# Optimization experiments

Hardware: AMD Instinct MI355X
Metric: run time of the kernel (lower is better)

Reference implementation:

```python
import jax, jax.numpy as jnp
import numpy as np

B, T, I, H, L, O = 256, 336, 16, 512, 256, 10


def setup_inputs() -> dict:
    key = jax.random.key(0)
    ks = jax.random.split(key, 24)
    n = lambda k, s, sc=1.0: jax.random.normal(k, s, dtype=jnp.float32) * sc
    mask = lambda k, s: (jax.random.uniform(k, s) > 0.5).astype(jnp.float32) * 2.0  # dropout p=0.5
    return {
        "x": n(ks[0], (B, T, I)),
        # dropout masks (inverted-dropout scaling already applied)
        "drop_x": mask(ks[1], (B, T, I)),
        "drop_h": mask(ks[2], (B, H)),
        "drop_l": mask(ks[3], (B, L)),
        # BayesianLSTM variational params + reparameterization noise
        "wih_mu": n(ks[4], (I, 4 * H), 0.05), "wih_rho": jnp.full((I, 4 * H), -5.0, jnp.float32), "eps_wih": n(ks[5], (I, 4 * H)),
        "whh_mu": n(ks[6], (H, 4 * H), 0.05), "whh_rho": jnp.full((H, 4 * H), -5.0, jnp.float32), "eps_whh": n(ks[7], (H, 4 * H)),
        "b_mu": n(ks[8], (4 * H,), 0.05), "b_rho": jnp.full((4 * H,), -5.0, jnp.float32), "eps_b": n(ks[9], (4 * H,)),
        # BayesianLinear variational params + noise (weight is [out, in])
        "blw_mu": n(ks[10], (L, H), 0.05), "blw_rho": jnp.full((L, H), -5.0, jnp.float32), "eps_blw": n(ks[11], (L, H)),
        "blb_mu": n(ks[12], (L,), 0.05), "blb_rho": jnp.full((L,), -5.0, jnp.float32), "eps_blb": n(ks[13], (L,)),
        # final deterministic linear, no bias
        "lin_w": n(ks[14], (O, L), 0.05),
    }


def _forward(x, drop_x, drop_h, drop_l,
             wih_mu, wih_rho, eps_wih, whh_mu, whh_rho, eps_whh,
             b_mu, b_rho, eps_b, blw_mu, blw_rho, eps_blw,
             blb_mu, blb_rho, eps_blb, lin_w):
    sp = jax.nn.softplus
    # sample weights: w = mu + softplus(rho) * eps
    Wih = wih_mu + sp(wih_rho) * eps_wih        # [I, 4H]
    Whh = whh_mu + sp(whh_rho) * eps_whh        # [H, 4H]
    b = b_mu + sp(b_rho) * eps_b                # [4H]
    BLW = blw_mu + sp(blw_rho) * eps_blw        # [L, H]
    BLb = blb_mu + sp(blb_rho) * eps_blb        # [L]

    xd = x * drop_x                             # dropout on input
    # precompute input-to-gate projection for all timesteps: [B, T, 4H]
    xg = jnp.einsum('bti,ig->btg', xd, Wih) + b

    def step(carry, xg_t):
        h, c = carry
        gates = xg_t + h @ Whh                  # [B, 4H]
        i, f, g, o = jnp.split(gates, 4, axis=-1)
        i = jax.nn.sigmoid(i)
        f = jax.nn.sigmoid(f)
        g = jnp.tanh(g)
        o = jax.nn.sigmoid(o)
        c = f * c + i * g
        h = o * jnp.tanh(c)
        return (h, c), h

    h0 = jnp.zeros((x.shape[0], Whh.shape[0]), x.dtype)
    (_, _), hs = jax.lax.scan(step, (h0, h0), jnp.swapaxes(xg, 0, 1))  # hs: [T, B, H]
    hidden_seq = jnp.swapaxes(hs, 0, 1)         # blitz returns batch-major [B, T, H]
    # faithful to lstm_out.view(sequence_length, len(x), hidden_dim)[-1] (reshape, not transpose)
    last = hidden_seq.reshape(T, x.shape[0], -1)[-1]    # [B, H]

    y = jax.nn.relu((last * drop_h) @ BLW.T + BLb)      # Bayesian linear + ReLU
    return (y * drop_l) @ lin_w.T                       # final linear, no bias


def reference(x, drop_x, drop_h, drop_l,
              wih_mu, wih_rho, eps_wih, whh_mu, whh_rho, eps_whh,
              b_mu, b_rho, eps_b, blw_mu, blw_rho, eps_blw,
              blb_mu, blb_rho, eps_blb, lin_w):
    return _forward(x, drop_x, drop_h, drop_l,
                    wih_mu, wih_rho, eps_wih, whh_mu, whh_rho, eps_whh,
                    b_mu, b_rho, eps_b, blw_mu, blw_rho, eps_blw,
                    blb_mu, blb_rho, eps_blb, lin_w)
```

## Files before the change

### kernel.cpp

```cpp
#include <hip/hip_runtime.h>
#include <hip/hip_fp16.h>

#define T_STEPS 336
#define NWG 32

typedef unsigned long long u64;

__device__ float g_h[337 * 512];
__device__ float g_blw[256 * 512];
__device__ float g_blb[256];
__device__ u64   g_hh[2][512];

__device__ __forceinline__ float softplus_f(float x) {
  return (x > 20.f) ? x : log1pf(__expf(x));
}
__device__ __forceinline__ float sigmoid_f(float x) {
  return 1.f / (1.f + __expf(-x));
}
__device__ __forceinline__ float tanh_f(float x) {
  x = fminf(fmaxf(x, -15.f), 15.f);
  float e = __expf(-2.f * x);
  return (1.f - e) / (1.f + e);
}

__global__ __launch_bounds__(256) void prep_kernel(
    const float* __restrict__ blw_mu, const float* __restrict__ blw_rho, const float* __restrict__ eps_blw,
    const float* __restrict__ blb_mu, const float* __restrict__ blb_rho, const float* __restrict__ eps_blb)
{
  const int bid = blockIdx.x, tid = threadIdx.x;
  if (bid < 512) {
    const int e = bid * 256 + tid;
    g_blw[e] = blw_mu[e] + softplus_f(blw_rho[e]) * eps_blw[e];
  } else {
    g_blb[tid] = blb_mu[tid] + softplus_f(blb_rho[tid]) * eps_blb[tid];
    u64* p = &g_hh[0][0];
    #pragma unroll
    for (int q = 0; q < 4; ++q)
      __hip_atomic_store(p + q * 256 + tid, 0ULL, __ATOMIC_RELAXED,
                         __HIP_MEMORY_SCOPE_AGENT);
  }
}

__global__ __launch_bounds__(512) void lstm_kernel(
    const float* __restrict__ x, const float* __restrict__ drop_x,
    const float* __restrict__ wih_mu, const float* __restrict__ wih_rho, const float* __restrict__ eps_wih,
    const float* __restrict__ b_mu, const float* __restrict__ b_rho, const float* __restrict__ eps_b,
    const float* __restrict__ whh_mu, const float* __restrict__ whh_rho, const float* __restrict__ eps_whh)
{
  const int r = blockIdx.x;
  const int tid = threadIdx.x;
  const int cl = tid & 63;
  const int seg = tid >> 6;
  const int gate = cl >> 4, kl = cl & 15;
  const int col = gate * 512 + r * 16 + kl;
  const int row0 = seg * 64;

  __shared__ float  xd[336 * 16];
  __shared__ __half hs16[512];
  __shared__ float  part[2][8][64];

  for (int e = tid; e < 5376; e += 512) {
    const int src = 255 * 5376 + e;
    xd[e] = x[src] * drop_x[src];
  }

  float w[64];
  #pragma unroll
  for (int j = 0; j < 64; ++j) {
    const int idx = (row0 + j) * 2048 + col;
    w[j] = whh_mu[idx] + softplus_f(whh_rho[idx]) * eps_whh[idx];
  }

  float wih[16];
  float bias = 0.f;
  if (tid < 64) {
    bias = b_mu[col] + softplus_f(b_rho[col]) * eps_b[col];
    #pragma unroll
    for (int i = 0; i < 16; ++i) {
      const int idx = i * 2048 + col;
      wih[i] = wih_mu[idx] + softplus_f(wih_rho[idx]) * eps_wih[idx];
    }
  }
  __syncthreads();

  auto xg_at = [&](int t) -> float {
    const float4* xr = (const float4*)(xd + t * 16);
    float4 x0 = xr[0], x1 = xr[1], x2 = xr[2], x3 = xr[3];
    float s0 = fmaf(x0.x, wih[0], bias);
    s0 = fmaf(x0.y, wih[1], s0); s0 = fmaf(x0.z, wih[2], s0); s0 = fmaf(x0.w, wih[3], s0);
    float s1 = x1.x * wih[4];
    s1 = fmaf(x1.y, wih[5], s1); s1 = fmaf(x1.z, wih[6], s1); s1 = fmaf(x1.w, wih[7], s1);
    float s2 = x2.x * wih[8];
    s2 = fmaf(x2.y, wih[9], s2); s2 = fmaf(x2.z, wih[10], s2); s2 = fmaf(x2.w, wih[11], s2);
    float s3 = x3.x * wih[12];
    s3 = fmaf(x3.y, wih[13], s3); s3 = fmaf(x3.z, wih[14], s3); s3 = fmaf(x3.w, wih[15], s3);
    return (s0 + s1) + (s2 + s3);
  };

  float c = 0.f;
  float xgv = (tid < 64) ? xg_at(0) : 0.f;

  for (int t = 0; t < T_STEPS; ++t) {
    const int p = t & 1;

    {
      const u64* slot = &g_hh[p][tid];
      u64 v;
      int it = 0;
      for (;;) {
        v = __hip_atomic_load(slot, __ATOMIC_RELAXED, __HIP_MEMORY_SCOPE_AGENT);
        if ((unsigned)(v >> 32) == (unsigned)t) break;
        if (++it > (1 << 20)) break;
      }
      hs16[tid] = __float2half(__uint_as_float((unsigned)v));
    }

    float a0 = 0.f, a1 = 0.f, a2 = 0.f, a3 = 0.f;
    const float4* hv = (const float4*)(hs16 + row0);
    #pragma unroll
    for (int jj = 0; jj < 8; ++jj) {
      float4 q = hv[jj];
      const __half2* hp = (const __half2*)&q;
      float2 f0 = __half22float2(hp[0]);
      float2 f1 = __half22float2(hp[1]);
      float2 f2 = __half22float2(hp[2]);
      float2 f3 = __half22float2(hp[3]);
      a0 = fmaf(f0.x, w[8 * jj],     a0);
      a1 = fmaf(f0.y, w[8 * jj + 1], a1);
      a2 = fmaf(f1.x, w[8 * jj + 2], a2);
      a3 = fmaf(f1.y, w[8 * jj + 3], a3);
      a0 = fmaf(f2.x, w[8 * jj + 4], a0);
      a1 = fmaf(f2.y, w[8 * jj + 5], a1);
      a2 = fmaf(f3.x, w[8 * jj + 6], a2);
      a3 = fmaf(f3.y, w[8 * jj + 7], a3);
    }
    part[p][seg][cl] = (a0 + a1) + (a2 + a3);
    __syncthreads();

    if (tid < 64) {
      float g = xgv
              + ((part[p][0][tid] + part[p][1][tid]) + (part[p][2][tid] + part[p][3][tid]))
              + ((part[p][4][tid] + part[p][5][tid]) + (part[p][6][tid] + part[p][7][tid]));
      const bool is_g = (gate == 2);
      float xin = is_g ? 2.f * fminf(fmaxf(g, -15.f), 15.f) : g;
      float s = sigmoid_f(xin);
      float act = is_g ? 2.f * s - 1.f : s;
      float vi = __shfl(act, kl);
      float vf = __shfl(act, kl + 16);
      float vg = __shfl(act, kl + 32);
      float vo = __shfl(act, kl + 48);
      if (tid < 16) {
        c = vf * c + vi * vg;
        float h = vo * tanh_f(c);
        const int idx = r * 16 + tid;
        u64 pv = (((u64)(unsigned)(t + 1)) << 32) | (u64)__float_as_uint(h);
        __hip_atomic_store(&g_hh[(t + 1) & 1][idx], pv,
                           __ATOMIC_RELAXED, __HIP_MEMORY_SCOPE_AGENT);
        g_h[(t + 1) * 512 + idx] = h;
      }
      if (t + 1 < T_STEPS) xgv = xg_at(t + 1);
    }
  }
}

__global__ __launch_bounds__(256) void head_kernel(
    const float* __restrict__ drop_h, const float* __restrict__ drop_l,
    const float* __restrict__ lin_w, float* __restrict__ out)
{
  const int j = blockIdx.x, tid = threadIdx.x;
  __shared__ float hd[512];
  __shared__ float y[256];

  for (int k = tid; k < 512; k += 256)
    hd[k] = g_h[(81 + j) * 512 + k] * drop_h[j * 512 + k];
  __syncthreads();

  {
    const int l = tid;
    float acc = g_blb[l];
    const float* wrow = g_blw + l * 512;
    #pragma unroll 8
    for (int k = 0; k < 512; ++k) acc = fmaf(hd[k], wrow[k], acc);
    acc = fmaxf(acc, 0.f);
    y[l] = acc * drop_l[j * 256 + l];
  }
  __syncthreads();

  if (tid < 10) {
    float acc = 0.f;
    const float* lrow = lin_w + tid * 256;
    #pragma unroll 8
    for (int l = 0; l < 256; ++l) acc = fmaf(y[l], lrow[l], acc);
    out[j * 10 + tid] = acc;
  }
}

extern "C" void kernel_launch(void* const* d_in, const int* in_sizes, int n_in,
                              void* d_out, int out_size, void* d_ws, size_t ws_size,
                              hipStream_t stream) {
  const float* x        = (const float*)d_in[0];
  const float* drop_x   = (const float*)d_in[1];
  const float* drop_h   = (const float*)d_in[2];
  const float* drop_l   = (const float*)d_in[3];
  const float* wih_mu   = (const float*)d_in[4];
  const float* wih_rho  = (const float*)d_in[5];
  const float* eps_wih  = (const float*)d_in[6];
  const float* whh_mu   = (const float*)d_in[7];
  const float* whh_rho  = (const float*)d_in[8];
  const float* eps_whh  = (const float*)d_in[9];
  const float* b_mu     = (const float*)d_in[10];
  const float* b_rho    = (const float*)d_in[11];
  const float* eps_b    = (const float*)d_in[12];
  const float* blw_mu   = (const float*)d_in[13];
  const float* blw_rho  = (const float*)d_in[14];
  const float* eps_blw  = (const float*)d_in[15];
  const float* blb_mu   = (const float*)d_in[16];
  const float* blb_rho  = (const float*)d_in[17];
  const float* eps_blb  = (const float*)d_in[18];
  const float* lin_w    = (const float*)d_in[19];

  prep_kernel<<<513, 256, 0, stream>>>(blw_mu, blw_rho, eps_blw,
                                       blb_mu, blb_rho, eps_blb);

  lstm_kernel<<<NWG, 512, 0, stream>>>(x, drop_x,
                                       wih_mu, wih_rho, eps_wih,
                                       b_mu, b_rho, eps_b,
                                       whh_mu, whh_rho, eps_whh);

  head_kernel<<<256, 256, 0, stream>>>(drop_h, drop_l, lin_w, (float*)d_out);
}
```

Before: 732.0 us.

## Pipeline spin-wait polling in inline asm and fold BLW sampling into LSTM

Replaces the scalar atomic-load spin loop with hand-written GCN assembly that keeps three outstanding global loads in flight, so each poll iteration overlaps memory latency instead of serialising load-compare. It also moves the BayesianLinear weight sampling from a large separate prep launch into the LSTM kernel's prologue, shrinking the init kernel to a single block. The inline asm clobbers fixed registers and uses cache-bypass loads, which adds fragility and extra memory traffic during polling.

```diff
diff --git a/kernel.cpp b/kernel.cpp
--- a/kernel.cpp
+++ b/kernel.cpp
@@ -23,29 +23,67 @@
   return (1.f - e) / (1.f + e);
 }
 
-__global__ __launch_bounds__(256) void prep_kernel(
-    const float* __restrict__ blw_mu, const float* __restrict__ blw_rho, const float* __restrict__ eps_blw,
-    const float* __restrict__ blb_mu, const float* __restrict__ blb_rho, const float* __restrict__ eps_blb)
+__device__ __forceinline__ unsigned poll_slot(const u64* slot, unsigned t) {
+  unsigned lo;
+  asm volatile(
+    "s_mov_b32 s22, 0x40000\n\t"
+    "global_load_dwordx2 v[60:61], %[p], off sc1\n\t"
+    "global_load_dwordx2 v[62:63], %[p], off sc1\n\t"
+    "global_load_dwordx2 v[64:65], %[p], off sc1\n\t"
+    "POLL%=:\n\t"
+    "s_sub_u32 s22, s22, 1\n\t"
+    "s_cbranch_scc1 DA%=\n\t"
+    "s_waitcnt vmcnt(2)\n\t"
+    "v_cmp_eq_u32 vcc, %[t], v61\n\t"
+    "s_not_b64 s[20:21], vcc\n\t"
+    "s_cbranch_scc0 DA%=\n\t"
+    "global_load_dwordx2 v[60:61], %[p], off sc1\n\t"
+    "s_waitcnt vmcnt(2)\n\t"
+    "v_cmp_eq_u32 vcc, %[t], v63\n\t"
+    "s_not_b64 s[20:21], vcc\n\t"
+    "s_cbranch_scc0 DB%=\n\t"
+    "global_load_dwordx2 v[62:63], %[p], off sc1\n\t"
+    "s_waitcnt vmcnt(2)\n\t"
+    "v_cmp_eq_u32 vcc, %[t], v65\n\t"
+    "s_not_b64 s[20:21], vcc\n\t"
+    "s_cbranch_scc0 DC%=\n\t"
+    "global_load_dwordx2 v[64:65], %[p], off sc1\n\t"
+    "s_branch POLL%=\n\t"
+    "DA%=:\n\t"
+    "v_mov_b32 %[lo], v60\n\t"
+    "s_branch DONE%=\n\t"
+    "DB%=:\n\t"
+    "v_mov_b32 %[lo], v62\n\t"
+    "s_branch DONE%=\n\t"
+    "DC%=:\n\t"
+    "v_mov_b32 %[lo], v64\n\t"
+    "DONE%=:\n\t"
+    "s_waitcnt vmcnt(0)"
+    : [lo] "=v"(lo)
+    : [p] "v"(slot), [t] "s"(t)
+    : "v60","v61","v62","v63","v64","v65","vcc","s20","s21","s22","memory");
+  return lo;
+}
+
+__global__ __launch_bounds__(256) void init_kernel(
+    const float* __restrict__ blb_mu, const float* __restrict__ blb_rho,
+    const float* __restrict__ eps_blb)
 {
-  const int bid = blockIdx.x, tid = threadIdx.x;
-  if (bid < 512) {
-    const int e = bid * 256 + tid;
-    g_blw[e] = blw_mu[e] + softplus_f(blw_rho[e]) * eps_blw[e];
-  } else {
-    g_blb[tid] = blb_mu[tid] + softplus_f(blb_rho[tid]) * eps_blb[tid];
-    u64* p = &g_hh[0][0];
-    #pragma unroll
-    for (int q = 0; q < 4; ++q)
-      __hip_atomic_store(p + q * 256 + tid, 0ULL, __ATOMIC_RELAXED,
-                         __HIP_MEMORY_SCOPE_AGENT);
-  }
+  const int tid = threadIdx.x;
+  g_blb[tid] = blb_mu[tid] + softplus_f(blb_rho[tid]) * eps_blb[tid];
+  u64* p = &g_hh[0][0];
+  #pragma unroll
+  for (int q = 0; q < 4; ++q)
+    __hip_atomic_store(p + q * 256 + tid, 0ULL, __ATOMIC_RELAXED,
+                       __HIP_MEMORY_SCOPE_AGENT);
 }
 
 __global__ __launch_bounds__(512) void lstm_kernel(
     const float* __restrict__ x, const float* __restrict__ drop_x,
     const float* __restrict__ wih_mu, const float* __restrict__ wih_rho, const float* __restrict__ eps_wih,
     const float* __restrict__ b_mu, const float* __restrict__ b_rho, const float* __restrict__ eps_b,
-    const float* __restrict__ whh_mu, const float* __restrict__ whh_rho, const float* __restrict__ eps_whh)
+    const float* __restrict__ whh_mu, const float* __restrict__ whh_rho, const float* __restrict__ eps_whh,
+    const float* __restrict__ blw_mu, const float* __restrict__ blw_rho, const float* __restrict__ eps_blw)
 {
   const int r = blockIdx.x;
   const int tid = threadIdx.x;
@@ -58,6 +96,15 @@
   __shared__ float  xd[336 * 16];
   __shared__ __half hs16[512];
   __shared__ float  part[2][8][64];
+
+  {
+    const int e0 = (r * 512 + tid) * 8;
+    #pragma unroll
+    for (int q = 0; q < 8; ++q) {
+      const int e = e0 + q;
+      g_blw[e] = blw_mu[e] + softplus_f(blw_rho[e]) * eps_blw[e];
+    }
+  }
 
   for (int e = tid; e < 5376; e += 512) {
     const int src = 255 * 5376 + e;
@@ -104,15 +151,8 @@
     const int p = t & 1;
 
     {
-      const u64* slot = &g_hh[p][tid];
-      u64 v;
-      int it = 0;
-      for (;;) {
-        v = __hip_atomic_load(slot, __ATOMIC_RELAXED, __HIP_MEMORY_SCOPE_AGENT);
-        if ((unsigned)(v >> 32) == (unsigned)t) break;
-        if (++it > (1 << 20)) break;
-      }
-      hs16[tid] = __float2half(__uint_as_float((unsigned)v));
+      unsigned bits = poll_slot(&g_hh[p][tid], (unsigned)t);
+      hs16[tid] = __float2half(__uint_as_float(bits));
     }
 
     float a0 = 0.f, a1 = 0.f, a2 = 0.f, a3 = 0.f;
@@ -219,13 +259,13 @@
   const float* eps_blb  = (const float*)d_in[18];
   const float* lin_w    = (const float*)d_in[19];
 
-  prep_kernel<<<513, 256, 0, stream>>>(blw_mu, blw_rho, eps_blw,
-                                       blb_mu, blb_rho, eps_blb);
+  init_kernel<<<1, 256, 0, stream>>>(blb_mu, blb_rho, eps_blb);
 
   lstm_kernel<<<NWG, 512, 0, stream>>>(x, drop_x,
                                        wih_mu, wih_rho, eps_wih,
                                        b_mu, b_rho, eps_b,
-                                       whh_mu, whh_rho, eps_whh);
+                                       whh_mu, whh_rho, eps_whh,
+                                       blw_mu, blw_rho, eps_blw);
 
   head_kernel<<<256, 256, 0, stream>>>(drop_h, drop_l, lin_w, (float*)d_out);
 }
```

After: 794.6 us. +8.6%, slower.
